# Optimization experiments

Hardware: AMD Instinct MI355X
Metric: run time of the kernel (lower is better)

## Reference

```python
import jax, jax.numpy as jnp
import numpy as np

N_NODES = 64000
N_GRAPHS = 128


def _sage_conv(x, edge_index, Wl, Wr, b):
    # PyG SAGEConv (mean aggregator): out = lin_l(mean_{j in N(i)} x_j) + lin_r(x_i)
    src, dst = edge_index[0], edge_index[1]
    msg = x[src]                                   # [E, d] gather
    s = jax.ops.segment_sum(msg, dst, num_segments=N_NODES)          # [N, d]
    cnt = jax.ops.segment_sum(jnp.ones(src.shape, x.dtype), dst,
                              num_segments=N_NODES)[:, None]          # [N, 1]
    aggr = jnp.where(cnt > 0, s / jnp.maximum(cnt, 1.0), jnp.zeros((), x.dtype))
    return aggr @ Wl.T + x @ Wr.T + b


def setup_inputs() -> dict:
    key = jax.random.key(0)
    ks = jax.random.split(key, 9)
    E = 1024000
    x = jax.random.normal(ks[0], (N_NODES, 64), dtype=jnp.float32)
    edge_index = jax.random.randint(ks[1], (2, E), 0, N_NODES, dtype=jnp.int64)
    batch = jnp.sort(jax.random.randint(ks[2], (N_NODES,), 0, N_GRAPHS, dtype=jnp.int64))
    sc = 1.0 / np.sqrt(64.0)
    Wl = jax.random.normal(ks[3], (3, 64, 64), dtype=jnp.float32) * sc
    Wr = jax.random.normal(ks[4], (3, 64, 64), dtype=jnp.float32) * sc
    b = jax.random.normal(ks[5], (3, 64), dtype=jnp.float32) * sc
    Wl_out = jax.random.normal(ks[6], (2, 64), dtype=jnp.float32) * sc
    Wr_out = jax.random.normal(ks[7], (2, 64), dtype=jnp.float32) * sc
    b_out = jax.random.normal(ks[8], (2,), dtype=jnp.float32) * sc
    return {"x": x, "edge_index": edge_index, "batch": batch,
            "Wl": Wl, "Wr": Wr, "b": b,
            "Wl_out": Wl_out, "Wr_out": Wr_out, "b_out": b_out}


def reference(x, edge_index, batch, Wl, Wr, b, Wl_out, Wr_out, b_out):
    h = x
    for i in range(Wl.shape[0]):  # fixed n_layers=3 hidden SAGEConv layers
        h = _sage_conv(h, edge_index, Wl[i], Wr[i], b[i])
        # dropout is identity at inference
        h = jax.nn.relu(h)
    h = _sage_conv(h, edge_index, Wl_out, Wr_out, b_out)  # [N, n_classes]
    # global mean pool over graphs in the batch
    s = jax.ops.segment_sum(h, batch, num_segments=N_GRAPHS)
    cnt = jax.ops.segment_sum(jnp.ones((N_NODES,), h.dtype), batch,
                              num_segments=N_GRAPHS)[:, None]
    return s / jnp.maximum(cnt, 1.0)
```

## Files before the change

### kernel.cpp

```cpp
#include <hip/hip_runtime.h>

#define NNODES 64000
#define NGRAPHS 128
#define D 64
#define NT 250
#define ESEG 5120
#define ZG 512

typedef _Float16 half8 __attribute__((ext_vector_type(8)));
typedef float f32x4 __attribute__((ext_vector_type(4)));

__device__ __forceinline__ int lower_bound(const int* __restrict__ a, int n, int key) {
    int lo = 0, hi = n;
    while (lo < hi) {
        int mid = (lo + hi) >> 1;
        if (a[mid] < key) lo = mid + 1; else hi = mid;
    }
    return lo;
}


__global__ void tohalf_kernel(const float4* __restrict__ x, half8* __restrict__ xh, int n8,
                              const float* __restrict__ Wl, const float* __restrict__ Wr,
                              _Float16* __restrict__ Wlh, _Float16* __restrict__ Wrh,
                              int* __restrict__ ecur) {
    int i = blockIdx.x * blockDim.x + threadIdx.x;
    int st = gridDim.x * blockDim.x;
    for (; i < n8; i += st) {
        float4 a = x[2 * i], b = x[2 * i + 1];
        half8 o;
        o[0] = (_Float16)a.x; o[1] = (_Float16)a.y; o[2] = (_Float16)a.z; o[3] = (_Float16)a.w;
        o[4] = (_Float16)b.x; o[5] = (_Float16)b.y; o[6] = (_Float16)b.z; o[7] = (_Float16)b.w;
        xh[i] = o;
    }
    int j = blockIdx.x * blockDim.x + threadIdx.x;
    if (j < 3 * D * D) {
        Wlh[j] = (_Float16)Wl[j];
        Wrh[j] = (_Float16)Wr[j];
    }
    if (blockIdx.x == 0 && threadIdx.x < 256) ecur[threadIdx.x] = 0;
}

__global__ __launch_bounds__(256) void partition_kernel(
        const int* __restrict__ src, const int* __restrict__ dst, int E,
        int* __restrict__ ecur, int2* __restrict__ elist) {
    __shared__ int bcnt[256], bbase[256];
    const int U = 8;
    int tid = threadIdx.x;
    for (int base = blockIdx.x * 256 * U; base < E; base += gridDim.x * 256 * U) {
        bcnt[tid] = 0;
        __syncthreads();
        int2 ed[U]; int team[U], slot[U];
#pragma unroll
        for (int u = 0; u < U; ++u) {
            int e = base + tid + u * 256;
            team[u] = -1;
            if (e < E) {
                int s = __builtin_nontemporal_load(src + e);
                int d = __builtin_nontemporal_load(dst + e);
                ed[u] = make_int2(s, d);
                team[u] = d >> 8;
                slot[u] = atomicAdd(&bcnt[team[u]], 1);
            }
        }
        __syncthreads();
        if (bcnt[tid] > 0) bbase[tid] = atomicAdd(&ecur[tid], bcnt[tid]);
        __syncthreads();
#pragma unroll
        for (int u = 0; u < U; ++u)
            if (team[u] >= 0)
                elist[(size_t)team[u] * ESEG + bbase[team[u]] + slot[u]] = ed[u];
        __syncthreads();
    }
}

__global__ __launch_bounds__(1024) void fill_block(
        const int2* __restrict__ elist, const int* __restrict__ ecur,
        const int* __restrict__ batch,
        int* __restrict__ offs, int2* __restrict__ info, int* __restrict__ col) {
    __shared__ int lhist[256], lofs[256];
    int team = blockIdx.x;
    int t = threadIdx.x;
    int n = ecur[team];
    const int2* el = elist + (size_t)team * ESEG;

    if (t < 256) lofs[t] = (t < NT) ? ecur[t] : 0;
    __syncthreads();
    for (int off = 1; off < 256; off <<= 1) {
        int x = 0;
        if (t < 256 && t >= off) x = lofs[t - off];
        __syncthreads();
        if (t < 256) lofs[t] += x;
        __syncthreads();
    }
    int tb = (team > 0) ? lofs[team - 1] : 0;
    if (team == NT - 1 && t == 0) offs[NNODES] = lofs[NT - 1];
    __syncthreads();

    if (t < 256) lhist[t] = 0;
    __syncthreads();
    for (int e = t; e < n; e += 1024)
        atomicAdd(&lhist[el[e].y & 255], 1);
    __syncthreads();
    if (t < 256) lofs[t] = lhist[t];
    __syncthreads();
    for (int off = 1; off < 256; off <<= 1) {
        int x = 0;
        if (t < 256 && t >= off) x = lofs[t - off];
        __syncthreads();
        if (t < 256) lofs[t] += x;
        __syncthreads();
    }
    if (t < 256) {
        int v = lhist[t];
        int ex = lofs[t] - v;
        int gi = team * 256 + t;
        offs[gi] = tb + ex;
        float inv = (v > 0) ? 1.f / (float)v : 0.f;
        info[gi] = make_int2(batch[gi], __float_as_int(inv));
        lofs[t] = ex;
    }
    __syncthreads();
    for (int e = t; e < n; e += 1024) {
        int2 ed = el[e];
        int p = tb + atomicAdd(&lofs[ed.y & 255], 1);
        col[p] = ed.x;
    }
}

template <int PRJ>
__global__ __launch_bounds__(256) void layer_fused(
        const _Float16* __restrict__ h, _Float16* __restrict__ out,
        const int* __restrict__ offs, const int* __restrict__ col,
        const _Float16* __restrict__ Wlh, const _Float16* __restrict__ Wrh,
        const float* __restrict__ b,
        const float* __restrict__ Wlo, const float* __restrict__ Wro,
        float* __restrict__ z12, float* __restrict__ z34) {
    __shared__ _Float16 tile[4][16][D];
    int lane = threadIdx.x & 63;
    int w    = threadIdx.x >> 6;
    int row0 = (blockIdx.x * 4 + w) * 16;

    int ns = lane >> 3;
    int ch = lane & 7;
#pragma unroll
    for (int pass = 0; pass < 2; ++pass) {
        int i = row0 + pass * 8 + ns;
        int beg = offs[i], end = offs[i + 1];
        half8 sa = {0, 0, 0, 0, 0, 0, 0, 0};
        int e = beg;
        for (; e + 8 <= end; e += 8) {
            int c[8];
#pragma unroll
            for (int u = 0; u < 8; ++u) c[u] = col[e + u];
            half8 v[8];
#pragma unroll
            for (int u = 0; u < 8; ++u)
                v[u] = *(const half8*)(h + (size_t)c[u] * D + ch * 8);
            half8 t0 = v[0] + v[1], t1 = v[2] + v[3];
            half8 t2 = v[4] + v[5], t3 = v[6] + v[7];
            sa += (t0 + t1) + (t2 + t3);
        }
        for (; e + 4 <= end; e += 4) {
            int c0 = col[e], c1 = col[e + 1], c2 = col[e + 2], c3 = col[e + 3];
            half8 v0 = *(const half8*)(h + (size_t)c0 * D + ch * 8);
            half8 v1 = *(const half8*)(h + (size_t)c1 * D + ch * 8);
            half8 v2 = *(const half8*)(h + (size_t)c2 * D + ch * 8);
            half8 v3 = *(const half8*)(h + (size_t)c3 * D + ch * 8);
            sa += (v0 + v1) + (v2 + v3);
        }
        for (; e < end; ++e)
            sa += *(const half8*)(h + (size_t)col[e] * D + ch * 8);
        float inv = (end > beg) ? 1.f / (float)(end - beg) : 0.f;
        half8 o;
#pragma unroll
        for (int j = 0; j < 8; ++j) o[j] = (_Float16)((float)sa[j] * inv);
        *(half8*)(&tile[w][pass * 8 + ns][ch * 8]) = o;
    }

    int r = lane & 15;
    int g = lane >> 4;

    half8 bf[4][4];
#pragma unroll
    for (int kt = 0; kt < 4; ++kt) {
        const _Float16* Wm = (kt < 2) ? Wlh : Wrh;
        int kk = (kt & 1) * 32 + g * 8;
#pragma unroll
        for (int nt = 0; nt < 4; ++nt)
            bf[kt][nt] = *(const half8*)(Wm + (size_t)(nt * 16 + r) * D + kk);
    }

    f32x4 acc[4];
#pragma unroll
    for (int nt = 0; nt < 4; ++nt) {
        float bv = b[nt * 16 + r];
        acc[nt] = (f32x4){bv, bv, bv, bv};
    }

#pragma unroll
    for (int kt = 0; kt < 4; ++kt) {
        int kk = (kt & 1) * 32 + g * 8;
        half8 af;
        if (kt < 2) af = *(const half8*)(&tile[w][r][kk]);
        else        af = *(const half8*)(h + (size_t)(row0 + r) * D + kk);
#pragma unroll
        for (int nt = 0; nt < 4; ++nt)
            acc[nt] = __builtin_amdgcn_mfma_f32_16x16x32_f16(af, bf[kt][nt], acc[nt], 0, 0, 0);
    }

    if (!PRJ) {
#pragma unroll
        for (int nt = 0; nt < 4; ++nt)
#pragma unroll
            for (int q = 0; q < 4; ++q) {
                int row = row0 + g * 4 + q;
                out[(size_t)row * D + nt * 16 + r] = (_Float16)fmaxf(acc[nt][q], 0.f);
            }
    } else {
#pragma unroll
        for (int nt = 0; nt < 4; ++nt)
#pragma unroll
            for (int q = 0; q < 4; ++q)
                tile[w][g * 4 + q][nt * 16 + r] = (_Float16)fmaxf(acc[nt][q], 0.f);

        half8 pf[2];
#pragma unroll
        for (int kt = 0; kt < 2; ++kt) {
            half8 t = {0, 0, 0, 0, 0, 0, 0, 0};
            if (r < 4) {
                const float* Pr = (r < 2) ? (Wlo + r * D) : (Wro + (r - 2) * D);
                int kk = kt * 32 + g * 8;
#pragma unroll
                for (int j = 0; j < 8; ++j) t[j] = (_Float16)Pr[kk + j];
            }
            pf[kt] = t;
        }
        f32x4 az = (f32x4){0.f, 0.f, 0.f, 0.f};
#pragma unroll
        for (int kt = 0; kt < 2; ++kt) {
            half8 af = *(const half8*)(&tile[w][r][kt * 32 + g * 8]);
            az = __builtin_amdgcn_mfma_f32_16x16x32_f16(af, pf[kt], az, 0, 0, 0);
        }
#pragma unroll
        for (int q = 0; q < 4; ++q) {
            int row = row0 + g * 4 + q;
            if (r < 2)      z12[row * 2 + r]       = az[q];
            else if (r < 4) z34[row * 2 + (r - 2)] = az[q];
        }
    }
}

__global__ __launch_bounds__(256) void zpool_edge(
        const float2* __restrict__ z12, const float2* __restrict__ z34,
        const int* __restrict__ src, const int* __restrict__ dst,
        const int2* __restrict__ info, int E, float* __restrict__ pbuf) {
    __shared__ float lp[NGRAPHS * 2];
    int t = threadIdx.x;
    lp[t] = 0.f;
    __syncthreads();
    int tid = blockIdx.x * blockDim.x + t;
    int stride = gridDim.x * blockDim.x;
    for (int e = tid; e < E; e += stride) {
        int s = __builtin_nontemporal_load(src + e);
        int d = __builtin_nontemporal_load(dst + e);
        float2 z = z12[s];
        int2 nf = info[d];
        float w = __int_as_float(nf.y);
        atomicAdd(&lp[nf.x * 2 + 0], z.x * w);
        atomicAdd(&lp[nf.x * 2 + 1], z.y * w);
    }
    for (int i = tid; i < NNODES; i += stride) {
        float2 zi = z34[i];
        int g = info[i].x;
        atomicAdd(&lp[g * 2 + 0], zi.x);
        atomicAdd(&lp[g * 2 + 1], zi.y);
    }
    __syncthreads();
    pbuf[blockIdx.x * (NGRAPHS * 2) + t] = lp[t];
}

__global__ void out_kernel(const float* __restrict__ pbuf, const int* __restrict__ batch,
                           const float* __restrict__ bo, float* __restrict__ out) {
    int t = threadIdx.x;
    float s = 0.f;
    for (int k = 0; k < ZG; ++k) s += pbuf[k * (NGRAPHS * 2) + t];
    int g = t >> 1, j = t & 1;
    int start = lower_bound(batch, NNODES, g);
    int end   = lower_bound(batch, NNODES, g + 1);
    int c = end - start;
    out[t] = (c > 0) ? s / (float)c + bo[j] : 0.f;
}


extern "C" void kernel_launch(void* const* d_in, const int* in_sizes, int n_in,
                              void* d_out, int out_size, void* d_ws, size_t ws_size,
                              hipStream_t stream) {
    const float* x    = (const float*)d_in[0];
    const int*   eidx = (const int*)d_in[1];
    const int*   batch= (const int*)d_in[2];
    const float* Wl   = (const float*)d_in[3];
    const float* Wr   = (const float*)d_in[4];
    const float* b    = (const float*)d_in[5];
    const float* Wlo  = (const float*)d_in[6];
    const float* Wro  = (const float*)d_in[7];
    const float* bo   = (const float*)d_in[8];

    int E = in_sizes[1] / 2;
    const int* src = eidx;
    const int* dst = eidx + E;

    char* ws = (char*)d_ws;
    size_t hb = (size_t)NNODES * D * 2;
    _Float16* xh   = (_Float16*)ws;
    _Float16* bufA = (_Float16*)(ws + hb);
    char* p = ws + 2 * hb;
    _Float16* Wlh  = (_Float16*)p;  p += 3 * D * D * 2;
    _Float16* Wrh  = (_Float16*)p;  p += 3 * D * D * 2;
    int*    col  = (int*)p;     p += (size_t)E * 4;
    int*    offs = (int*)p;     p += ((size_t)(NNODES + 1) * 4 + 127) / 128 * 128;
    int2*   info = (int2*)p;    p += (size_t)NNODES * 8;
    float*  z12  = (float*)p;   p += (size_t)NNODES * 8;
    float*  z34  = (float*)p;   p += (size_t)NNODES * 8;
    int*    ecur = (int*)p;     p += 1024;
    float*  pbuf = (float*)p;   p += (size_t)ZG * NGRAPHS * 2 * 4;
    int2*   elist= (int2*)p;

    tohalf_kernel<<<2000, 256, 0, stream>>>((const float4*)x, (half8*)xh, NNODES * D / 8,
                                            Wl, Wr, Wlh, Wrh, ecur);

    partition_kernel<<<512, 256, 0, stream>>>(src, dst, E, ecur, elist);
    fill_block<<<NT, 1024, 0, stream>>>(elist, ecur, batch, offs, info, col);

    layer_fused<0><<<1000, 256, 0, stream>>>(xh,   bufA, offs, col,
                                             Wlh,             Wrh,             b,
                                             nullptr, nullptr, nullptr, nullptr);
    layer_fused<0><<<1000, 256, 0, stream>>>(bufA, xh,   offs, col,
                                             Wlh + D * D,     Wrh + D * D,     b + D,
                                             nullptr, nullptr, nullptr, nullptr);
    layer_fused<1><<<1000, 256, 0, stream>>>(xh,   bufA, offs, col,
                                             Wlh + 2 * D * D, Wrh + 2 * D * D, b + 2 * D,
                                             Wlo, Wro, z12, z34);

    zpool_edge<<<ZG, 256, 0, stream>>>((const float2*)z12, (const float2*)z34,
                                       src, dst, info, E, pbuf);
    out_kernel<<<1, 256, 0, stream>>>(pbuf, batch, bo, (float*)d_out);
}
```

Baseline: 151.6 us.

## Merge conversion into partition, halve rows per wave, fold final reduction

Fuses the fp16 conversion and the edge partition into one launch by splitting blocks between the two roles, and replaces the ecur reset with a memset. Layer kernels now aggregate 8 rows per wave instead of 16 and launch twice as many blocks, so more waves are in flight to hide gather latency. The price is that the 16-row MFMA tile is half padding. The final out_kernel is folded into zpool_edge through a last-block-done atomic counter, removing one launch but adding a threadfence and a serial reduction in one block.

New measurement: 217.4 us. 43.5% more time.

```diff
diff --git a/kernel.cpp b/kernel.cpp
--- a/kernel.cpp
+++ b/kernel.cpp
@@ -6,6 +6,8 @@
 #define NT 250
 #define ESEG 5120
 #define ZG 512
+#define PGRID 512
+#define CGRID 2000
 
 typedef _Float16 half8 __attribute__((ext_vector_type(8)));
 typedef float f32x4 __attribute__((ext_vector_type(4)));
@@ -19,58 +21,57 @@
     return lo;
 }
 
-
-__global__ void tohalf_kernel(const float4* __restrict__ x, half8* __restrict__ xh, int n8,
-                              const float* __restrict__ Wl, const float* __restrict__ Wr,
-                              _Float16* __restrict__ Wlh, _Float16* __restrict__ Wrh,
-                              int* __restrict__ ecur) {
-    int i = blockIdx.x * blockDim.x + threadIdx.x;
-    int st = gridDim.x * blockDim.x;
-    for (; i < n8; i += st) {
-        float4 a = x[2 * i], b = x[2 * i + 1];
-        half8 o;
-        o[0] = (_Float16)a.x; o[1] = (_Float16)a.y; o[2] = (_Float16)a.z; o[3] = (_Float16)a.w;
-        o[4] = (_Float16)b.x; o[5] = (_Float16)b.y; o[6] = (_Float16)b.z; o[7] = (_Float16)b.w;
-        xh[i] = o;
-    }
-    int j = blockIdx.x * blockDim.x + threadIdx.x;
-    if (j < 3 * D * D) {
-        Wlh[j] = (_Float16)Wl[j];
-        Wrh[j] = (_Float16)Wr[j];
-    }
-    if (blockIdx.x == 0 && threadIdx.x < 256) ecur[threadIdx.x] = 0;
-}
-
-__global__ __launch_bounds__(256) void partition_kernel(
+__global__ __launch_bounds__(256) void convert_partition(
+        const float4* __restrict__ x, half8* __restrict__ xh, int n8,
+        const float* __restrict__ Wl, const float* __restrict__ Wr,
+        _Float16* __restrict__ Wlh, _Float16* __restrict__ Wrh,
         const int* __restrict__ src, const int* __restrict__ dst, int E,
         int* __restrict__ ecur, int2* __restrict__ elist) {
     __shared__ int bcnt[256], bbase[256];
-    const int U = 8;
     int tid = threadIdx.x;
-    for (int base = blockIdx.x * 256 * U; base < E; base += gridDim.x * 256 * U) {
-        bcnt[tid] = 0;
-        __syncthreads();
-        int2 ed[U]; int team[U], slot[U];
-#pragma unroll
-        for (int u = 0; u < U; ++u) {
-            int e = base + tid + u * 256;
-            team[u] = -1;
-            if (e < E) {
-                int s = __builtin_nontemporal_load(src + e);
-                int d = __builtin_nontemporal_load(dst + e);
-                ed[u] = make_int2(s, d);
-                team[u] = d >> 8;
-                slot[u] = atomicAdd(&bcnt[team[u]], 1);
+    if (blockIdx.x < PGRID) {
+        const int U = 8;
+        for (int base = blockIdx.x * 256 * U; base < E; base += PGRID * 256 * U) {
+            bcnt[tid] = 0;
+            __syncthreads();
+            int2 ed[U]; int team[U], slot[U];
+#pragma unroll
+            for (int u = 0; u < U; ++u) {
+                int e = base + tid + u * 256;
+                team[u] = -1;
+                if (e < E) {
+                    int s = __builtin_nontemporal_load(src + e);
+                    int d = __builtin_nontemporal_load(dst + e);
+                    ed[u] = make_int2(s, d);
+                    team[u] = d >> 8;
+                    slot[u] = atomicAdd(&bcnt[team[u]], 1);
+                }
             }
-        }
-        __syncthreads();
-        if (bcnt[tid] > 0) bbase[tid] = atomicAdd(&ecur[tid], bcnt[tid]);
-        __syncthreads();
-#pragma unroll
-        for (int u = 0; u < U; ++u)
-            if (team[u] >= 0)
-                elist[(size_t)team[u] * ESEG + bbase[team[u]] + slot[u]] = ed[u];
-        __syncthreads();
+            __syncthreads();
+            if (bcnt[tid] > 0) bbase[tid] = atomicAdd(&ecur[tid], bcnt[tid]);
+            __syncthreads();
+#pragma unroll
+            for (int u = 0; u < U; ++u)
+                if (team[u] >= 0)
+                    elist[(size_t)team[u] * ESEG + bbase[team[u]] + slot[u]] = ed[u];
+            __syncthreads();
+        }
+    } else {
+        int bid = blockIdx.x - PGRID;
+        int i = bid * 256 + tid;
+        int st = CGRID * 256;
+        for (; i < n8; i += st) {
+            float4 a = x[2 * i], b = x[2 * i + 1];
+            half8 o;
+            o[0] = (_Float16)a.x; o[1] = (_Float16)a.y; o[2] = (_Float16)a.z; o[3] = (_Float16)a.w;
+            o[4] = (_Float16)b.x; o[5] = (_Float16)b.y; o[6] = (_Float16)b.z; o[7] = (_Float16)b.w;
+            xh[i] = o;
+        }
+        int j = bid * 256 + tid;
+        if (j < 3 * D * D) {
+            Wlh[j] = (_Float16)Wl[j];
+            Wrh[j] = (_Float16)Wr[j];
+        }
     }
 }
 
@@ -139,13 +140,14 @@
     __shared__ _Float16 tile[4][16][D];
     int lane = threadIdx.x & 63;
     int w    = threadIdx.x >> 6;
-    int row0 = (blockIdx.x * 4 + w) * 16;
-
+    int row0 = (blockIdx.x * 4 + w) * 8;
     int ns = lane >> 3;
     int ch = lane & 7;
-#pragma unroll
-    for (int pass = 0; pass < 2; ++pass) {
-        int i = row0 + pass * 8 + ns;
+
+    *(half8*)(&tile[w][8 + ns][ch * 8]) = (half8){0, 0, 0, 0, 0, 0, 0, 0};
+
+    {
+        int i = row0 + ns;
         int beg = offs[i], end = offs[i + 1];
         half8 sa = {0, 0, 0, 0, 0, 0, 0, 0};
         int e = beg;
@@ -175,7 +177,7 @@
         half8 o;
 #pragma unroll
         for (int j = 0; j < 8; ++j) o[j] = (_Float16)((float)sa[j] * inv);
-        *(half8*)(&tile[w][pass * 8 + ns][ch * 8]) = o;
+        *(half8*)(&tile[w][ns][ch * 8]) = o;
     }
 
     int r = lane & 15;
@@ -198,32 +200,37 @@
         acc[nt] = (f32x4){bv, bv, bv, bv};
     }
 
+    int srow = row0 + r;
+    if (srow >= NNODES) srow = NNODES - 1;
 #pragma unroll
     for (int kt = 0; kt < 4; ++kt) {
         int kk = (kt & 1) * 32 + g * 8;
         half8 af;
         if (kt < 2) af = *(const half8*)(&tile[w][r][kk]);
-        else        af = *(const half8*)(h + (size_t)(row0 + r) * D + kk);
+        else        af = *(const half8*)(h + (size_t)srow * D + kk);
 #pragma unroll
         for (int nt = 0; nt < 4; ++nt)
             acc[nt] = __builtin_amdgcn_mfma_f32_16x16x32_f16(af, bf[kt][nt], acc[nt], 0, 0, 0);
     }
 
     if (!PRJ) {
-#pragma unroll
-        for (int nt = 0; nt < 4; ++nt)
-#pragma unroll
-            for (int q = 0; q < 4; ++q) {
-                int row = row0 + g * 4 + q;
-                out[(size_t)row * D + nt * 16 + r] = (_Float16)fmaxf(acc[nt][q], 0.f);
-            }
+        if (g < 2) {
+#pragma unroll
+            for (int nt = 0; nt < 4; ++nt)
+#pragma unroll
+                for (int q = 0; q < 4; ++q) {
+                    int row = row0 + g * 4 + q;
+                    out[(size_t)row * D + nt * 16 + r] = (_Float16)fmaxf(acc[nt][q], 0.f);
+                }
+        }
     } else {
-#pragma unroll
-        for (int nt = 0; nt < 4; ++nt)
-#pragma unroll
-            for (int q = 0; q < 4; ++q)
-                tile[w][g * 4 + q][nt * 16 + r] = (_Float16)fmaxf(acc[nt][q], 0.f);
-
+        if (g < 2) {
+#pragma unroll
+            for (int nt = 0; nt < 4; ++nt)
+#pragma unroll
+                for (int q = 0; q < 4; ++q)
+                    tile[w][g * 4 + q][nt * 16 + r] = (_Float16)fmaxf(acc[nt][q], 0.f);
+        }
         half8 pf[2];
 #pragma unroll
         for (int kt = 0; kt < 2; ++kt) {
@@ -242,11 +249,13 @@
             half8 af = *(const half8*)(&tile[w][r][kt * 32 + g * 8]);
             az = __builtin_amdgcn_mfma_f32_16x16x32_f16(af, pf[kt], az, 0, 0, 0);
         }
-#pragma unroll
-        for (int q = 0; q < 4; ++q) {
-            int row = row0 + g * 4 + q;
-            if (r < 2)      z12[row * 2 + r]       = az[q];
-            else if (r < 4) z34[row * 2 + (r - 2)] = az[q];
+        if (g < 2) {
+#pragma unroll
+            for (int q = 0; q < 4; ++q) {
+                int row = row0 + g * 4 + q;
+                if (r < 2)      z12[row * 2 + r]       = az[q];
+                else if (r < 4) z34[row * 2 + (r - 2)] = az[q];
+            }
         }
     }
 }
@@ -254,8 +263,11 @@
 __global__ __launch_bounds__(256) void zpool_edge(
         const float2* __restrict__ z12, const float2* __restrict__ z34,
         const int* __restrict__ src, const int* __restrict__ dst,
-        const int2* __restrict__ info, int E, float* __restrict__ pbuf) {
+        const int2* __restrict__ info, int E, float* __restrict__ pbuf,
+        int* __restrict__ done, const int* __restrict__ batch,
+        const float* __restrict__ bo, float* __restrict__ outp) {
     __shared__ float lp[NGRAPHS * 2];
+    __shared__ int isLast;
     int t = threadIdx.x;
     lp[t] = 0.f;
     __syncthreads();
@@ -278,18 +290,18 @@
     }
     __syncthreads();
     pbuf[blockIdx.x * (NGRAPHS * 2) + t] = lp[t];
-}
-
-__global__ void out_kernel(const float* __restrict__ pbuf, const int* __restrict__ batch,
-                           const float* __restrict__ bo, float* __restrict__ out) {
-    int t = threadIdx.x;
-    float s = 0.f;
-    for (int k = 0; k < ZG; ++k) s += pbuf[k * (NGRAPHS * 2) + t];
-    int g = t >> 1, j = t & 1;
-    int start = lower_bound(batch, NNODES, g);
-    int end   = lower_bound(batch, NNODES, g + 1);
-    int c = end - start;
-    out[t] = (c > 0) ? s / (float)c + bo[j] : 0.f;
+    __threadfence();
+    __syncthreads();
+    if (t == 0) isLast = (atomicAdd(done, 1) == ZG - 1);
+    __syncthreads();
+    if (isLast) {
+        __threadfence();
+        float s = 0.f;
+        for (int k = 0; k < ZG; ++k) s += pbuf[k * (NGRAPHS * 2) + t];
+        int g = t >> 1, j = t & 1;
+        int c = lower_bound(batch, NNODES, g + 1) - lower_bound(batch, NNODES, g);
+        outp[t] = (c > 0) ? s / (float)c + bo[j] : 0.f;
+    }
 }
 
 
@@ -323,26 +335,29 @@
     float*  z12  = (float*)p;   p += (size_t)NNODES * 8;
     float*  z34  = (float*)p;   p += (size_t)NNODES * 8;
     int*    ecur = (int*)p;     p += 1024;
+    int*    done = (int*)p;     p += 1024;
     float*  pbuf = (float*)p;   p += (size_t)ZG * NGRAPHS * 2 * 4;
     int2*   elist= (int2*)p;
 
-    tohalf_kernel<<<2000, 256, 0, stream>>>((const float4*)x, (half8*)xh, NNODES * D / 8,
-                                            Wl, Wr, Wlh, Wrh, ecur);
-
-    partition_kernel<<<512, 256, 0, stream>>>(src, dst, E, ecur, elist);
+    hipMemsetAsync(ecur, 0, 1024 + sizeof(int), stream);
+
+    convert_partition<<<PGRID + CGRID, 256, 0, stream>>>(
+        (const float4*)x, (half8*)xh, NNODES * D / 8,
+        Wl, Wr, Wlh, Wrh, src, dst, E, ecur, elist);
+
     fill_block<<<NT, 1024, 0, stream>>>(elist, ecur, batch, offs, info, col);
 
-    layer_fused<0><<<1000, 256, 0, stream>>>(xh,   bufA, offs, col,
+    layer_fused<0><<<2000, 256, 0, stream>>>(xh,   bufA, offs, col,
                                              Wlh,             Wrh,             b,
                                              nullptr, nullptr, nullptr, nullptr);
-    layer_fused<0><<<1000, 256, 0, stream>>>(bufA, xh,   offs, col,
+    layer_fused<0><<<2000, 256, 0, stream>>>(bufA, xh,   offs, col,
                                              Wlh + D * D,     Wrh + D * D,     b + D,
                                              nullptr, nullptr, nullptr, nullptr);
-    layer_fused<1><<<1000, 256, 0, stream>>>(xh,   bufA, offs, col,
+    layer_fused<1><<<2000, 256, 0, stream>>>(xh,   bufA, offs, col,
                                              Wlh + 2 * D * D, Wrh + 2 * D * D, b + 2 * D,
                                              Wlo, Wro, z12, z34);
 
     zpool_edge<<<ZG, 256, 0, stream>>>((const float2*)z12, (const float2*)z34,
-                                       src, dst, info, E, pbuf);
-    out_kernel<<<1, 256, 0, stream>>>(pbuf, batch, bo, (float*)d_out);
-}
+                                       src, dst, info, E, pbuf,
+                                       done, batch, bo, (float*)d_out);
+}
```
